# Optimization experiments

Measured on AMD Instinct MI355X. Metric: run time of the kernel, lower is better.

## Reference

```python
import jax, jax.numpy as jnp
import numpy as np

N_NODES = 100000
IN_CH = 65
HID_CH = 64
N_EDGES = 3200000


def setup_inputs() -> dict:
    key = jax.random.key(0)
    k1, k2, k3, k4, k5 = jax.random.split(key, 5)
    x = jax.random.normal(k1, (N_NODES, IN_CH), dtype=jnp.float32)
    edge_index = jax.random.randint(k2, (2, N_EDGES), 0, N_NODES, dtype=jnp.int64)
    edge_weight = jax.random.uniform(k3, (N_EDGES,), dtype=jnp.float32)
    # PyG GraphConv params: lin_rel (with bias) applied to aggregated neighbors,
    # lin_root (no bias) applied to self features.
    scale = 1.0 / np.sqrt(IN_CH)
    W_rel = jax.random.uniform(k4, (HID_CH, IN_CH), dtype=jnp.float32, minval=-scale, maxval=scale)
    b_rel = jnp.zeros((HID_CH,), dtype=jnp.float32)
    W_root = jax.random.uniform(k5, (HID_CH, IN_CH), dtype=jnp.float32, minval=-scale, maxval=scale)
    return {"x": x, "edge_index": edge_index, "edge_weight": edge_weight,
            "W_rel": W_rel, "b_rel": b_rel, "W_root": W_root}


def reference(x, edge_index, edge_weight, W_rel, b_rel, W_root):
    src = edge_index[0]  # source nodes (x_j in PyG message)
    dst = edge_index[1]  # target nodes (aggregation index)
    # gather neighbor features, weight by edge weight: [E, IN_CH]
    msgs = x[src] * edge_weight[:, None]
    # scatter-add to destination nodes: [N, IN_CH]
    aggr = jax.ops.segment_sum(msgs, dst, num_segments=N_NODES)
    # out = lin_rel(aggr) + lin_root(x)
    out = aggr @ W_rel.T + b_rel + x @ W_root.T
    return out
```

## Files before the change

kernel.cpp:

```cpp
#include <hip/hip_runtime.h>

#define IN_CH 65
#define HID 64
#define BN 64
#define NB 1563
#define CAP 2560
#define SCAP 2432
#define EPB 16384
#define TPS 1024
#define EPT (EPB / TPS)
#define WSTR 132

static inline size_t align16(size_t v) { return (v + 15) & ~(size_t)15; }

__device__ inline ushort f2bf(float f) {
    uint u = __float_as_uint(f);
    return (ushort)((u + 0x7FFF + ((u >> 16) & 1)) >> 16);
}

__global__ __launch_bounds__(256) void k1both(const float* __restrict__ x,
                                              const float* __restrict__ W_rel,
                                              const float* __restrict__ W_root,
                                              const float* __restrict__ b_rel,
                                              ushort* __restrict__ y16,
                                              float* __restrict__ out,
                                              int* __restrict__ cnt, int nBuckets,
                                              int nNodes) {
    __shared__ float xsT[65 * 68];
    __shared__ float ws[65 * 136];
    const int tid = threadIdx.x;
    const int tx = tid & 15;
    const int ty = tid >> 4;
    const long nodeBase = (long)blockIdx.x * 64;
    const int nValid = (int)min((long)64, (long)nNodes - nodeBase);

    if (cnt && tid == 0 && blockIdx.x < (unsigned)nBuckets) cnt[blockIdx.x] = 0;

    for (int f = tid; f < HID * IN_CH; f += 256) {
        const int j = f / IN_CH, c = f - j * IN_CH;
        ws[c * 136 + j] = W_rel[f];
    }
    for (int f = tid; f < HID * IN_CH; f += 256) {
        const int j = f / IN_CH, c = f - j * IN_CH;
        ws[c * 136 + 68 + j] = W_root[f];
    }
    const float* xsrc = x + nodeBase * IN_CH;
    for (int f = tid; f < 64 * IN_CH; f += 256) {
        const int node = f / IN_CH, k = f - node * IN_CH;
        xsT[k * 68 + node] = (node < nValid) ? xsrc[f] : 0.f;
    }
    __syncthreads();

    float acc[4][8];
#pragma unroll
    for (int i = 0; i < 4; ++i)
#pragma unroll
        for (int j = 0; j < 8; ++j) acc[i][j] = 0.f;

    const int r0 = ty * 4;
    const int isRoot = tx >> 3;
    const int c0 = (tx & 7) * 8;
    const int wofs = isRoot * 68 + c0;

    for (int k = 0; k < IN_CH; ++k) {
        const float4 a4 = *(const float4*)&xsT[k * 68 + r0];
        const float4 b0 = *(const float4*)&ws[k * 136 + wofs];
        const float4 b1 = *(const float4*)&ws[k * 136 + wofs + 4];
        const float aa[4] = {a4.x, a4.y, a4.z, a4.w};
        const float bb[8] = {b0.x, b0.y, b0.z, b0.w, b1.x, b1.y, b1.z, b1.w};
#pragma unroll
        for (int i = 0; i < 4; ++i)
#pragma unroll
            for (int j = 0; j < 8; ++j) acc[i][j] += aa[i] * bb[j];
    }

    if (isRoot) {
        const float4 bb0 = *(const float4*)&b_rel[c0];
        const float4 bb1 = *(const float4*)&b_rel[c0 + 4];
        const float bv[8] = {bb0.x, bb0.y, bb0.z, bb0.w, bb1.x, bb1.y, bb1.z, bb1.w};
#pragma unroll
        for (int i = 0; i < 4; ++i)
#pragma unroll
            for (int j = 0; j < 8; ++j) acc[i][j] += bv[j];
    }

#pragma unroll
    for (int i = 0; i < 4; ++i) {
        const long node = nodeBase + r0 + i;
        if (node >= nNodes) break;
        if (!isRoot) {
            uint4 pk;
            pk.x = (uint)f2bf(acc[i][0]) | ((uint)f2bf(acc[i][1]) << 16);
            pk.y = (uint)f2bf(acc[i][2]) | ((uint)f2bf(acc[i][3]) << 16);
            pk.z = (uint)f2bf(acc[i][4]) | ((uint)f2bf(acc[i][5]) << 16);
            pk.w = (uint)f2bf(acc[i][6]) | ((uint)f2bf(acc[i][7]) << 16);
            *(uint4*)&y16[node * HID + c0] = pk;
        } else {
            float* dst = out + node * HID + c0;
            *(float4*)(dst + 0) = make_float4(acc[i][0], acc[i][1], acc[i][2], acc[i][3]);
            *(float4*)(dst + 4) = make_float4(acc[i][4], acc[i][5], acc[i][6], acc[i][7]);
        }
    }
}

__global__ __launch_bounds__(TPS) void scatterB(const int* __restrict__ ei,
                                                const float* __restrict__ ew,
                                                int* __restrict__ cnt,
                                                int2* __restrict__ pairs, int E) {
    __shared__ int lhist[NB];
    __shared__ int lbase[NB];
    const int tid = threadIdx.x;
    const long e0 = (long)blockIdx.x * EPB;
    const int n = (int)min((long)EPB, (long)E - e0);

    for (int i = tid; i < NB; i += TPS) lhist[i] = 0;
    __syncthreads();

    int dstv[EPT], srcv[EPT];
    float wv[EPT];
#pragma unroll
    for (int k = 0; k < EPT; ++k) {
        const int i = tid + k * TPS;
        const bool valid = i < n;
        dstv[k] = valid ? ei[(long)E + e0 + i] : 0;
        srcv[k] = valid ? ei[e0 + i] : 0;
        wv[k]   = valid ? ew[e0 + i] : 0.f;
        if (valid) atomicAdd(&lhist[dstv[k] >> 6], 1);
    }
    __syncthreads();

    for (int i = tid; i < NB; i += TPS) {
        const int c = lhist[i];
        lbase[i] = c ? atomicAdd(&cnt[i], c) : 0;
        lhist[i] = 0;
    }
    __syncthreads();

#pragma unroll
    for (int k = 0; k < EPT; ++k) {
        const int i = tid + k * TPS;
        if (i < n) {
            const int b = dstv[k] >> 6;
            const int p = lbase[b] + atomicAdd(&lhist[b], 1);
            if (p < CAP)
                pairs[(size_t)b * CAP + p] =
                    make_int2((srcv[k] << 7) | ((dstv[k] & (BN - 1)) << 25),
                              __float_as_int(wv[k]));
        }
    }
}

__global__ __launch_bounds__(512) void aggregateS16(const int2* __restrict__ pairs,
                                                    const int* __restrict__ cnt,
                                                    const ushort* __restrict__ y16,
                                                    float* __restrict__ out, int N) {
    __shared__ int2 sorted[SCAP];
    __shared__ int sH[BN];
    __shared__ int soff[BN + 1];
    __shared__ int scur[BN];
    const int tid = threadIdx.x;
    const int lane = tid & 63;
    const int wvid = tid >> 6;
    const int half = lane >> 5;
    const uint lane4 = (lane & 31) * 4;
    const int b = blockIdx.x;

    if (tid < BN) { sH[tid] = 0; scur[tid] = 0; }

    const int m = min(cnt[b], CAP);
    const int2* pb = pairs + (size_t)b * CAP;

    int2 pv[5];
#pragma unroll
    for (int kk = 0; kk < 5; ++kk) {
        const int i = tid + kk * 512;
        if (i < m) pv[kk] = pb[i];
    }
    __syncthreads();

#pragma unroll
    for (int kk = 0; kk < 5; ++kk) {
        const int i = tid + kk * 512;
        if (i < m) atomicAdd(&sH[(uint)pv[kk].x >> 25], 1);
    }
    __syncthreads();

    for (int off = 1; off < BN; off <<= 1) {
        int v = 0;
        if (tid < BN) {
            v = sH[tid];
            if (tid >= off) v += sH[tid - off];
        }
        __syncthreads();
        if (tid < BN) sH[tid] = v;
        __syncthreads();
    }
    if (tid < BN) soff[tid + 1] = sH[tid];
    if (tid == 0) soff[0] = 0;
    __syncthreads();

#pragma unroll
    for (int kk = 0; kk < 5; ++kk) {
        const int i = tid + kk * 512;
        if (i < m) {
            const int d = (uint)pv[kk].x >> 25;
            const int slot = soff[d] + atomicAdd(&scur[d], 1);
            if (slot < SCAP) sorted[slot] = make_int2(pv[kk].x & 0x00FFFF80, pv[kk].y);
        }
    }
    __syncthreads();

    const char* yb = (const char*)y16;
    const long nodeBase = (long)b * BN;
    for (int nl = wvid; nl < BN; nl += 8) {
        const long node = nodeBase + nl;
        if (node >= N) break;
        const int kbeg = min(soff[nl], SCAP);
        const int kend = min(soff[nl + 1], SCAP);
        float2* o = (float2*)(out + node * HID) + (lane & 31);
        const float2 cur = *o;
        float ax = 0.f, ay = 0.f;
        int k = kbeg + half;
        for (; k + 14 < kend; k += 16) {
            int2 pp[8];
#pragma unroll
            for (int j = 0; j < 8; ++j) pp[j] = sorted[k + 2 * j];
            uint qq[8];
#pragma unroll
            for (int j = 0; j < 8; ++j)
                qq[j] = *(const uint*)(yb + (uint)pp[j].x + lane4);
#pragma unroll
            for (int j = 0; j < 8; ++j) {
                const float w = __int_as_float(pp[j].y);
                ax += w * __uint_as_float(qq[j] << 16);
                ay += w * __uint_as_float(qq[j] & 0xFFFF0000u);
            }
        }
        for (; k + 6 < kend; k += 8) {
            const int2 p0 = sorted[k],     p1 = sorted[k + 2];
            const int2 p2 = sorted[k + 4], p3 = sorted[k + 6];
            const uint q0 = *(const uint*)(yb + (uint)p0.x + lane4);
            const uint q1 = *(const uint*)(yb + (uint)p1.x + lane4);
            const uint q2 = *(const uint*)(yb + (uint)p2.x + lane4);
            const uint q3 = *(const uint*)(yb + (uint)p3.x + lane4);
            const float w0 = __int_as_float(p0.y), w1 = __int_as_float(p1.y);
            const float w2 = __int_as_float(p2.y), w3 = __int_as_float(p3.y);
            ax += w0 * __uint_as_float(q0 << 16);
            ay += w0 * __uint_as_float(q0 & 0xFFFF0000u);
            ax += w1 * __uint_as_float(q1 << 16);
            ay += w1 * __uint_as_float(q1 & 0xFFFF0000u);
            ax += w2 * __uint_as_float(q2 << 16);
            ay += w2 * __uint_as_float(q2 & 0xFFFF0000u);
            ax += w3 * __uint_as_float(q3 << 16);
            ay += w3 * __uint_as_float(q3 & 0xFFFF0000u);
        }
        for (; k < kend; k += 2) {
            const int2 p = sorted[k];
            const uint q = *(const uint*)(yb + (uint)p.x + lane4);
            const float w = __int_as_float(p.y);
            ax += w * __uint_as_float(q << 16);
            ay += w * __uint_as_float(q & 0xFFFF0000u);
        }
        ax += __shfl_xor(ax, 32);
        ay += __shfl_xor(ay, 32);
        if (half == 0) {
            *o = make_float2(cur.x + ax, cur.y + ay);
        }
    }
}

__global__ __launch_bounds__(256) void k1_full(const float* __restrict__ x,
                                               const float* __restrict__ W_rel,
                                               const float* __restrict__ b_rel,
                                               const float* __restrict__ W_root,
                                               ushort* __restrict__ y16,
                                               float* __restrict__ out,
                                               int nNodes) {
    __shared__ float xs[64 * IN_CH];
    __shared__ float ws[IN_CH * WSTR];
    const int tid = threadIdx.x;
    const int tx = tid & 15;
    const int ty = tid >> 4;
    const long nodeBase = (long)blockIdx.x * 64;
    const int nValid = min(64, nNodes - (int)nodeBase);
    const int nx = nValid * IN_CH;

    for (int f = tid; f < HID * IN_CH; f += 256) {
        const int j = f / IN_CH, c = f - j * IN_CH;
        ws[c * WSTR + j] = W_rel[f];
    }
    for (int f = tid; f < HID * IN_CH; f += 256) {
        const int j = f / IN_CH, c = f - j * IN_CH;
        ws[c * WSTR + HID + j] = W_root[f];
    }
    const float* xsrc = x + nodeBase * IN_CH;
    for (int i = tid; i < 64 * IN_CH; i += 256) xs[i] = (i < nx) ? xsrc[i] : 0.f;
    __syncthreads();

    float acc[4][8];
#pragma unroll
    for (int i = 0; i < 4; ++i)
#pragma unroll
        for (int j = 0; j < 8; ++j) acc[i][j] = 0.f;

    const int r0 = ty * 4;
    const int c0 = tx * 8;
    for (int k = 0; k < IN_CH; ++k) {
        float aa[4] = {xs[(r0 + 0) * IN_CH + k], xs[(r0 + 1) * IN_CH + k],
                       xs[(r0 + 2) * IN_CH + k], xs[(r0 + 3) * IN_CH + k]};
        float4 b0 = *(const float4*)&ws[k * WSTR + c0];
        float4 b1 = *(const float4*)&ws[k * WSTR + c0 + 4];
        float bb[8] = {b0.x, b0.y, b0.z, b0.w, b1.x, b1.y, b1.z, b1.w};
#pragma unroll
        for (int i = 0; i < 4; ++i)
#pragma unroll
            for (int j = 0; j < 8; ++j) acc[i][j] += aa[i] * bb[j];
    }

    if (c0 >= HID) {
        const int h0 = c0 - HID;
        float4 bb0 = *(const float4*)&b_rel[h0];
        float4 bb1 = *(const float4*)&b_rel[h0 + 4];
        float bv[8] = {bb0.x, bb0.y, bb0.z, bb0.w, bb1.x, bb1.y, bb1.z, bb1.w};
#pragma unroll
        for (int i = 0; i < 4; ++i)
#pragma unroll
            for (int j = 0; j < 8; ++j) acc[i][j] += bv[j];
    }

#pragma unroll
    for (int i = 0; i < 4; ++i) {
        const long node = nodeBase + r0 + i;
        if (node >= nNodes) break;
        if (c0 < HID) {
            uint4 pk;
            pk.x = (uint)f2bf(acc[i][0]) | ((uint)f2bf(acc[i][1]) << 16);
            pk.y = (uint)f2bf(acc[i][2]) | ((uint)f2bf(acc[i][3]) << 16);
            pk.z = (uint)f2bf(acc[i][4]) | ((uint)f2bf(acc[i][5]) << 16);
            pk.w = (uint)f2bf(acc[i][6]) | ((uint)f2bf(acc[i][7]) << 16);
            *(uint4*)&y16[node * HID + c0] = pk;
        } else {
            float* dst = out + node * HID + (c0 - HID);
            *(float4*)(dst + 0) = make_float4(acc[i][0], acc[i][1], acc[i][2], acc[i][3]);
            *(float4*)(dst + 4) = make_float4(acc[i][4], acc[i][5], acc[i][6], acc[i][7]);
        }
    }
}

__global__ __launch_bounds__(256) void k2_atomic16(const int* __restrict__ ei,
                                                   const float* __restrict__ ew,
                                                   const ushort* __restrict__ y16,
                                                   float* __restrict__ out, int E) {
    const long t = (long)blockIdx.x * 256 + threadIdx.x;
    const long e = t >> 4;
    const int r = (int)(t & 15);
    if (e >= E) return;
    const int src = ei[e];
    const int dst = ei[(long)E + e];
    const float w = ew[e];
    const uint2 q = ((const uint2*)y16)[(size_t)src * 16 + r];
    float* o = out + (size_t)dst * HID + r * 4;
    unsafeAtomicAdd(o + 0, w * __uint_as_float(q.x << 16));
    unsafeAtomicAdd(o + 1, w * __uint_as_float(q.x & 0xFFFF0000u));
    unsafeAtomicAdd(o + 2, w * __uint_as_float(q.y << 16));
    unsafeAtomicAdd(o + 3, w * __uint_as_float(q.y & 0xFFFF0000u));
}

extern "C" void kernel_launch(void* const* d_in, const int* in_sizes, int n_in,
                              void* d_out, int out_size, void* d_ws, size_t ws_size,
                              hipStream_t stream) {
    const float* x      = (const float*)d_in[0];
    const int*   ei     = (const int*)d_in[1];
    const float* ew     = (const float*)d_in[2];
    const float* W_rel  = (const float*)d_in[3];
    const float* b_rel  = (const float*)d_in[4];
    const float* W_root = (const float*)d_in[5];
    float* out = (float*)d_out;

    const int N = in_sizes[0] / IN_CH;
    const int E = in_sizes[2];

    char* base = (char*)d_ws;
    const size_t oY     = 0;
    const size_t oPairs = align16((size_t)N * HID * 2);
    const size_t oCnt   = oPairs + align16((size_t)NB * CAP * 8);
    const size_t need   = oCnt + (size_t)NB * 4;

    ushort* y16 = (ushort*)(base + oY);
    const int nb1 = (N + 63) / 64;

    const bool fits = (ws_size >= need) && (N <= (1 << 17)) &&
                      ((size_t)NB * BN >= (size_t)N) && ((long)E <= (long)N * 33) &&
                      (nb1 >= NB);

    if (fits) {
        int2* pairs = (int2*)(base + oPairs);
        int*  cnt   = (int*)(base + oCnt);

        k1both<<<nb1, 256, 0, stream>>>(x, W_rel, W_root, b_rel, y16, out, cnt, NB, N);
        scatterB<<<(E + EPB - 1) / EPB, TPS, 0, stream>>>(ei, ew, cnt, pairs, E);
        aggregateS16<<<NB, 512, 0, stream>>>(pairs, cnt, y16, out, N);
    } else {
        const int nbf = (N + 63) / 64;
        k1_full<<<nbf, 256, 0, stream>>>(x, W_rel, b_rel, W_root, y16, out, N);
        const long thr2 = (long)E * 16;
        k2_atomic16<<<(int)((thr2 + 255) / 256), 256, 0, stream>>>(ei, ew, y16, out, E);
    }
}
```

Measured before the change: 244.1 us.

## Split dense GEMM into two passes, wave-shuffle prefix scan, deeper gather unroll

The first kernel now computes the W_rel and W_root products in two sequential passes that reuse one weight tile in shared memory. This halves weight LDS and per-thread accumulators, which should raise occupancy, at the cost of an extra barrier and a second weight load. The per-bucket 64-entry prefix scan is replaced by a single-wave shuffle scan, removing the barrier loop. The gather loop's main unroll goes from 8 to 16 pairs per iteration to keep more loads in flight, which raises register pressure.

```diff
diff --git a/kernel.cpp b/kernel.cpp
--- a/kernel.cpp
+++ b/kernel.cpp
@@ -27,7 +27,7 @@
                                               int* __restrict__ cnt, int nBuckets,
                                               int nNodes) {
     __shared__ float xsT[65 * 68];
-    __shared__ float ws[65 * 136];
+    __shared__ float ws[65 * 68];
     const int tid = threadIdx.x;
     const int tx = tid & 15;
     const int ty = tid >> 4;
@@ -38,11 +38,7 @@
 
     for (int f = tid; f < HID * IN_CH; f += 256) {
         const int j = f / IN_CH, c = f - j * IN_CH;
-        ws[c * 136 + j] = W_rel[f];
-    }
-    for (int f = tid; f < HID * IN_CH; f += 256) {
-        const int j = f / IN_CH, c = f - j * IN_CH;
-        ws[c * 136 + 68 + j] = W_root[f];
+        ws[c * 68 + j] = W_rel[f];
     }
     const float* xsrc = x + nodeBase * IN_CH;
     for (int f = tid; f < 64 * IN_CH; f += 256) {
@@ -51,54 +47,68 @@
     }
     __syncthreads();
 
-    float acc[4][8];
-#pragma unroll
-    for (int i = 0; i < 4; ++i)
-#pragma unroll
-        for (int j = 0; j < 8; ++j) acc[i][j] = 0.f;
-
     const int r0 = ty * 4;
-    const int isRoot = tx >> 3;
-    const int c0 = (tx & 7) * 8;
-    const int wofs = isRoot * 68 + c0;
-
-    for (int k = 0; k < IN_CH; ++k) {
-        const float4 a4 = *(const float4*)&xsT[k * 68 + r0];
-        const float4 b0 = *(const float4*)&ws[k * 136 + wofs];
-        const float4 b1 = *(const float4*)&ws[k * 136 + wofs + 4];
-        const float aa[4] = {a4.x, a4.y, a4.z, a4.w};
-        const float bb[8] = {b0.x, b0.y, b0.z, b0.w, b1.x, b1.y, b1.z, b1.w};
+    const int c0 = tx * 4;
+
+    {
+        float acc[4][4];
 #pragma unroll
         for (int i = 0; i < 4; ++i)
 #pragma unroll
-            for (int j = 0; j < 8; ++j) acc[i][j] += aa[i] * bb[j];
-    }
-
-    if (isRoot) {
-        const float4 bb0 = *(const float4*)&b_rel[c0];
-        const float4 bb1 = *(const float4*)&b_rel[c0 + 4];
-        const float bv[8] = {bb0.x, bb0.y, bb0.z, bb0.w, bb1.x, bb1.y, bb1.z, bb1.w};
-#pragma unroll
-        for (int i = 0; i < 4; ++i)
-#pragma unroll
-            for (int j = 0; j < 8; ++j) acc[i][j] += bv[j];
-    }
-
-#pragma unroll
-    for (int i = 0; i < 4; ++i) {
-        const long node = nodeBase + r0 + i;
-        if (node >= nNodes) break;
-        if (!isRoot) {
-            uint4 pk;
+            for (int j = 0; j < 4; ++j) acc[i][j] = 0.f;
+
+        for (int k = 0; k < IN_CH; ++k) {
+            const float4 a4 = *(const float4*)&xsT[k * 68 + r0];
+            const float4 b4 = *(const float4*)&ws[k * 68 + c0];
+            const float aa[4] = {a4.x, a4.y, a4.z, a4.w};
+            const float bb[4] = {b4.x, b4.y, b4.z, b4.w};
+#pragma unroll
+            for (int i = 0; i < 4; ++i)
+#pragma unroll
+                for (int j = 0; j < 4; ++j) acc[i][j] += aa[i] * bb[j];
+        }
+#pragma unroll
+        for (int i = 0; i < 4; ++i) {
+            const long node = nodeBase + r0 + i;
+            if (node >= nNodes) break;
+            uint2 pk;
             pk.x = (uint)f2bf(acc[i][0]) | ((uint)f2bf(acc[i][1]) << 16);
             pk.y = (uint)f2bf(acc[i][2]) | ((uint)f2bf(acc[i][3]) << 16);
-            pk.z = (uint)f2bf(acc[i][4]) | ((uint)f2bf(acc[i][5]) << 16);
-            pk.w = (uint)f2bf(acc[i][6]) | ((uint)f2bf(acc[i][7]) << 16);
-            *(uint4*)&y16[node * HID + c0] = pk;
-        } else {
-            float* dst = out + node * HID + c0;
-            *(float4*)(dst + 0) = make_float4(acc[i][0], acc[i][1], acc[i][2], acc[i][3]);
-            *(float4*)(dst + 4) = make_float4(acc[i][4], acc[i][5], acc[i][6], acc[i][7]);
+            *(uint2*)&y16[node * HID + c0] = pk;
+        }
+    }
+    __syncthreads();
+
+    for (int f = tid; f < HID * IN_CH; f += 256) {
+        const int j = f / IN_CH, c = f - j * IN_CH;
+        ws[c * 68 + j] = W_root[f];
+    }
+    __syncthreads();
+
+    {
+        const float4 bb4 = *(const float4*)&b_rel[c0];
+        float acc[4][4];
+#pragma unroll
+        for (int i = 0; i < 4; ++i) {
+            acc[i][0] = bb4.x; acc[i][1] = bb4.y;
+            acc[i][2] = bb4.z; acc[i][3] = bb4.w;
+        }
+        for (int k = 0; k < IN_CH; ++k) {
+            const float4 a4 = *(const float4*)&xsT[k * 68 + r0];
+            const float4 b4 = *(const float4*)&ws[k * 68 + c0];
+            const float aa[4] = {a4.x, a4.y, a4.z, a4.w};
+            const float bb[4] = {b4.x, b4.y, b4.z, b4.w};
+#pragma unroll
+            for (int i = 0; i < 4; ++i)
+#pragma unroll
+                for (int j = 0; j < 4; ++j) acc[i][j] += aa[i] * bb[j];
+        }
+#pragma unroll
+        for (int i = 0; i < 4; ++i) {
+            const long node = nodeBase + r0 + i;
+            if (node >= nNodes) break;
+            *(float4*)&out[node * HID + c0] =
+                make_float4(acc[i][0], acc[i][1], acc[i][2], acc[i][3]);
         }
     }
 }
@@ -185,18 +195,16 @@
     }
     __syncthreads();
 
-    for (int off = 1; off < BN; off <<= 1) {
-        int v = 0;
-        if (tid < BN) {
-            v = sH[tid];
-            if (tid >= off) v += sH[tid - off];
-        }
-        __syncthreads();
-        if (tid < BN) sH[tid] = v;
-        __syncthreads();
-    }
-    if (tid < BN) soff[tid + 1] = sH[tid];
-    if (tid == 0) soff[0] = 0;
+    if (tid < BN) {
+        int v = sH[tid];
+#pragma unroll
+        for (int off = 1; off < BN; off <<= 1) {
+            const int u = __shfl_up(v, off);
+            if (lane >= off) v += u;
+        }
+        soff[tid + 1] = v;
+        if (tid == 0) soff[0] = 0;
+    }
     __syncthreads();
 
 #pragma unroll
@@ -221,16 +229,16 @@
         const float2 cur = *o;
         float ax = 0.f, ay = 0.f;
         int k = kbeg + half;
-        for (; k + 14 < kend; k += 16) {
-            int2 pp[8];
-#pragma unroll
-            for (int j = 0; j < 8; ++j) pp[j] = sorted[k + 2 * j];
-            uint qq[8];
-#pragma unroll
-            for (int j = 0; j < 8; ++j)
+        for (; k + 30 < kend; k += 32) {
+            int2 pp[16];
+#pragma unroll
+            for (int j = 0; j < 16; ++j) pp[j] = sorted[k + 2 * j];
+            uint qq[16];
+#pragma unroll
+            for (int j = 0; j < 16; ++j)
                 qq[j] = *(const uint*)(yb + (uint)pp[j].x + lane4);
 #pragma unroll
-            for (int j = 0; j < 8; ++j) {
+            for (int j = 0; j < 16; ++j) {
                 const float w = __int_as_float(pp[j].y);
                 ax += w * __uint_as_float(qq[j] << 16);
                 ay += w * __uint_as_float(qq[j] & 0xFFFF0000u);
```

Result: no change. 239.6 us (-1.8%).
